# Kernel optimization log

Measured on AMD Instinct MI355X. Metric: run time of the kernel, lower is better.

## Reference

```python
import jax, jax.numpy as jnp
import numpy as np

HEADS = 4
DIM_HEAD = 32
DIM = 128
HIDDEN = HEADS * DIM_HEAD  # 128
SCALE = DIM_HEAD ** -0.5


def setup_inputs() -> dict:
    key = jax.random.key(0)
    ks = jax.random.split(key, 7)
    b, c, h, w = 4, DIM, 256, 256
    x = jax.random.normal(ks[0], (b, c, h, w), dtype=jnp.float32)
    context = jax.random.normal(ks[1], (b, c, h, w), dtype=jnp.float32)
    # conv1x1 weights stored as [out, in] matrices
    s_in = 1.0 / np.sqrt(DIM)
    Wq = jax.random.uniform(ks[2], (HIDDEN, DIM), jnp.float32, -s_in, s_in)
    Wk = jax.random.uniform(ks[3], (HIDDEN, DIM), jnp.float32, -s_in, s_in)
    Wv = jax.random.uniform(ks[4], (HIDDEN, DIM), jnp.float32, -s_in, s_in)
    s_h = 1.0 / np.sqrt(HIDDEN)
    Wo = jax.random.uniform(ks[5], (DIM, HIDDEN), jnp.float32, -s_h, s_h)
    bo = jax.random.uniform(ks[6], (DIM,), jnp.float32, -s_h, s_h)
    return {"x": x, "context": context, "Wq": Wq, "Wk": Wk, "Wv": Wv, "Wo": Wo, "bo": bo}


def reference(x, context, Wq, Wk, Wv, Wo, bo):
    b, c, h, w = x.shape
    n = h * w
    xf = x.reshape(b, c, n)         # flatten spatial
    cf = context.reshape(b, c, n)
    # conv1x1 projections == channel matmuls
    q = jnp.einsum('oc,bcn->bon', Wq, xf).reshape(b, HEADS, DIM_HEAD, n)
    k = jnp.einsum('oc,bcn->bon', Wk, cf).reshape(b, HEADS, DIM_HEAD, n)
    v = jnp.einsum('oc,bcn->bon', Wv, cf).reshape(b, HEADS, DIM_HEAD, n)
    q = q * SCALE
    k = jax.nn.softmax(k, axis=-1)  # softmax over spatial positions
    ctx = jnp.einsum('bhdn,bhen->bhde', k, v)   # [b,h,d,e] small d_head x d_head
    out = jnp.einsum('bhde,bhdn->bhen', ctx, q)  # [b,h,e,n]
    out = out.reshape(b, HIDDEN, n)
    out = jnp.einsum('oc,bcn->bon', Wo, out) + bo[None, :, None]
    return out.reshape(b, c, h, w)
```

## Files before the change

### kernel.cpp

```cpp
#include <hip/hip_runtime.h>
#include <cstdint>
#include <cstddef>

typedef __bf16 bf16x8 __attribute__((ext_vector_type(8)));
typedef float f32x4 __attribute__((ext_vector_type(4)));
typedef unsigned int u32x4 __attribute__((ext_vector_type(4)));
typedef unsigned int u32x2 __attribute__((ext_vector_type(2)));

#define MFMA16(a, b, c) __builtin_amdgcn_mfma_f32_16x16x32_bf16((a), (b), (c), 0, 0, 0)

static constexpr int CD = 128;
static constexpr int NTOK = 65536;
static constexpr float F_SCALE = 0.17677669529663688f;
static constexpr float F_LOG2E = 1.4426950408889634f;
static constexpr int PART = 4224;

__device__ __forceinline__ void gload_lds16(const float* g, void* l) {
  __builtin_amdgcn_global_load_lds(
      (const __attribute__((address_space(1))) void*)g,
      (__attribute__((address_space(3))) void*)l, 16, 0, 0);
}

__device__ __forceinline__ unsigned short bfb(float f) {
  return __builtin_bit_cast(unsigned short, (__bf16)f);
}
__device__ __forceinline__ unsigned pk2(float a, float b) {
  return (unsigned)bfb(a) | ((unsigned)bfb(b) << 16);
}

__device__ __forceinline__ void stage_swz(const float* src_base, float* T1,
                                          int w, int lg, int l15) {
#pragma unroll
  for (int i = 0; i < 8; ++i) {
    int c0 = w * 32 + i * 4;
    int row = c0 + lg;
    int g = l15 ^ ((row >> 3) & 3);
    gload_lds16(src_base + (size_t)row * NTOK + g * 4, (void*)(T1 + c0 * 64));
  }
}

__device__ __forceinline__ void transpose_vec(const float* T1, char* T2, int tid) {
  const int co = tid >> 4;
  const int nq = tid & 15;
  const int lgl = co & 3;
  f32x4 M[8];
#pragma unroll
  for (int i = 0; i < 8; ++i)
    M[i] = *(const f32x4*)(T1 + (co * 8 + i) * 64 + ((nq ^ lgl) * 4));
#pragma unroll
  for (int j = 0; j < 4; ++j) {
    int n = nq * 4 + j;
    u32x4 pk;
#pragma unroll
    for (int p = 0; p < 4; ++p)
      pk[p] = pk2(M[2 * p][j], M[2 * p + 1][j]);
    *(u32x4*)(T2 + n * 256 + ((co * 16) ^ ((n & 7) << 4))) = pk;
  }
}

__global__ __launch_bounds__(256, 2) void k1_ctx(
    const float* __restrict__ ctx_in, const float* __restrict__ Wk,
    const float* __restrict__ Wv, float* __restrict__ S_part,
    int cpb_log2, int nstrips) {
  __shared__ char smem[80 * 1024];
  float* T1 = (float*)smem;
  char* T2 = smem + 32 * 1024;
  char* EV = smem + 48 * 1024;

  const int tid = threadIdx.x;
  const int lane = tid & 63;
  const int w = tid >> 6;
  const int l15 = lane & 15;
  const int lg = lane >> 4;
  const int b = blockIdx.x >> cpb_log2;
  const int cb = blockIdx.x & ((1 << cpb_log2) - 1);

  bf16x8 Wf[4][4];
#pragma unroll
  for (int m = 0; m < 4; ++m) {
    const float* Wp = (m < 2) ? Wk : Wv;
    const float sc = (m < 2) ? F_LOG2E : 1.0f;
    int row = w * 32 + (m & 1) * 16 + l15;
#pragma unroll
    for (int ks = 0; ks < 4; ++ks) {
      const float* p = Wp + row * CD + ks * 32 + lg * 8;
#pragma unroll
      for (int e = 0; e < 8; ++e) Wf[m][ks][e] = (__bf16)(p[e] * sc);
    }
  }

  f32x4 Sacc[2][2];
#pragma unroll
  for (int i = 0; i < 2; ++i)
#pragma unroll
    for (int j = 0; j < 2; ++j) Sacc[i][j] = f32x4{0.f, 0.f, 0.f, 0.f};
  float zacc[2] = {0.f, 0.f};

  const float* src0 = ctx_in + (size_t)b * CD * NTOK + (size_t)cb * (nstrips * 64);
  const int xorr = (l15 & 7) << 4;
  char* Ew = EV + w * 8192;
  char* Vw = EV + w * 8192 + 4096;

  stage_swz(src0, T1, w, lg, l15);

  for (int s = 0; s < nstrips; ++s) {
    asm volatile("s_waitcnt vmcnt(0)" ::: "memory");
    __syncthreads();
    transpose_vec(T1, T2, tid);
    __syncthreads();
    if (s + 1 < nstrips) stage_swz(src0 + (s + 1) * 64, T1, w, lg, l15);

    f32x4 acc[4][4];
#pragma unroll
    for (int m = 0; m < 4; ++m)
#pragma unroll
      for (int t = 0; t < 4; ++t) acc[m][t] = f32x4{0.f, 0.f, 0.f, 0.f};
#pragma unroll
    for (int ks = 0; ks < 4; ++ks) {
      bf16x8 At[4];
#pragma unroll
      for (int t = 0; t < 4; ++t) {
        int n = t * 16 + l15;
        At[t] = *(const bf16x8*)(T2 + n * 256 + ((ks * 64 + lg * 16) ^ xorr));
      }
#pragma unroll
      for (int m = 0; m < 4; ++m)
#pragma unroll
        for (int t = 0; t < 4; ++t) acc[m][t] = MFMA16(At[t], Wf[m][ks], acc[m][t]);
    }

#pragma unroll
    for (int m = 0; m < 2; ++m) {
      int d = m * 16 + l15;
      int dx = (d & 7) << 4;
#pragma unroll
      for (int t = 0; t < 4; ++t) {
        f32x4 a = acc[m][t];
        float e0 = __builtin_exp2f(a[0]), e1 = __builtin_exp2f(a[1]);
        float e2 = __builtin_exp2f(a[2]), e3 = __builtin_exp2f(a[3]);
        zacc[m] += (e0 + e1) + (e2 + e3);
        u32x2 pe{pk2(e0, e1), pk2(e2, e3)};
        *(u32x2*)(Ew + d * 128 + ((t * 32 + lg * 8) ^ dx)) = pe;
        f32x4 v = acc[m + 2][t];
        u32x2 pv{pk2(v[0], v[1]), pk2(v[2], v[3])};
        *(u32x2*)(Vw + d * 128 + ((t * 32 + lg * 8) ^ dx)) = pv;
      }
    }

#pragma unroll
    for (int s2 = 0; s2 < 2; ++s2) {
      bf16x8 Ea[2], Vb[2];
#pragma unroll
      for (int md = 0; md < 2; ++md) {
        int d = md * 16 + l15;
        int off = (s2 * 64 + lg * 16) ^ ((d & 7) << 4);
        Ea[md] = *(const bf16x8*)(Ew + d * 128 + off);
        Vb[md] = *(const bf16x8*)(Vw + d * 128 + off);
      }
#pragma unroll
      for (int md = 0; md < 2; ++md)
#pragma unroll
        for (int ne = 0; ne < 2; ++ne) Sacc[md][ne] = MFMA16(Ea[md], Vb[ne], Sacc[md][ne]);
    }
  }

  float* outp = S_part + (size_t)blockIdx.x * PART;
#pragma unroll
  for (int md = 0; md < 2; ++md)
#pragma unroll
    for (int ne = 0; ne < 2; ++ne) {
      int e = ne * 16 + l15, d0 = md * 16 + lg * 4;
      *(f32x4*)(outp + w * 1024 + e * 32 + d0) = Sacc[md][ne];
    }
#pragma unroll
  for (int m = 0; m < 2; ++m) {
    float z = zacc[m];
    z += __shfl_xor(z, 16, 64);
    z += __shfl_xor(z, 32, 64);
    if (lg == 0) outp[4096 + w * 32 + m * 16 + l15] = z;
  }
}

__global__ void k2a_reduce(const float* __restrict__ S_part, float* __restrict__ S_red,
                           float* __restrict__ Z_red, int nparts) {
  int bid = blockIdx.x;
  int b = bid / 33, bs = bid % 33;
  int tid = threadIdx.x;
  __shared__ float red[256];
  int e_loc = tid & 127, half = tid >> 7;
  const float* base =
      S_part + (size_t)b * nparts * PART + (bs < 32 ? bs * 128 + e_loc : 4096 + e_loc);
  float sum = 0.f;
  int h = nparts >> 1;
  for (int p = half * h; p < half * h + h; ++p) sum += base[(size_t)p * PART];
  red[tid] = sum;
  __syncthreads();
  if (tid < 128) {
    float v = red[tid] + red[tid + 128];
    if (bs < 32)
      S_red[b * 4096 + bs * 128 + tid] = v;
    else
      Z_red[b * 128 + tid] = v;
  }
}

__global__ void k2b_weff(const float* __restrict__ S_red, const float* __restrict__ Z_red,
                         const float* __restrict__ Wq, const float* __restrict__ Wo,
                         float* __restrict__ W_eff) {
  int b = blockIdx.x >> 3, og = blockIdx.x & 7;
  int tid = threadIdx.x;
  __shared__ float ctx_lds[4096];
  __shared__ float T_lds[16 * 128];
  for (int i = tid * 16; i < tid * 16 + 16; ++i) {
    int hh = i >> 10, dd = i & 31;
    ctx_lds[i] = S_red[b * 4096 + i] / Z_red[b * 128 + hh * 32 + dd];
  }
  __syncthreads();
  {
    int o_loc = tid >> 4, hd0 = (tid & 15) * 8;
    int o = og * 16 + o_loc;
    for (int j = 0; j < 8; ++j) {
      int hd = hd0 + j, h = hd >> 5, d = hd & 31;
      const float* wo = Wo + o * 128 + h * 32;
      const float* cx = ctx_lds + h * 1024 + d;
      float acc = 0.f;
      for (int e = 0; e < 32; ++e) acc += wo[e] * cx[e * 32];
      T_lds[o_loc * 128 + hd] = acc;
    }
  }
  __syncthreads();
  {
    int o_loc = tid >> 4, c0 = (tid & 15) * 8;
    float acc[8] = {};
    const float* Trow = T_lds + o_loc * 128;
    for (int hd = 0; hd < 128; ++hd) {
      float tv = Trow[hd];
      const float* wq = Wq + hd * 128 + c0;
#pragma unroll
      for (int j = 0; j < 8; ++j) acc[j] += tv * wq[j];
    }
    float* op = W_eff + b * 16384 + (og * 16 + o_loc) * 128 + c0;
#pragma unroll
    for (int j = 0; j < 8; ++j) op[j] = F_SCALE * acc[j];
  }
}

__global__ __launch_bounds__(256, 3) void k3_out(const float* __restrict__ x,
                                                 const float* __restrict__ W_eff,
                                                 const float* __restrict__ bo,
                                                 float* __restrict__ out) {
  __shared__ char smem[48 * 1024];
  float* T1 = (float*)smem;
  char* T2 = smem + 32 * 1024;
  const int tid = threadIdx.x;
  const int lane = tid & 63;
  const int w = tid >> 6;
  const int l15 = lane & 15;
  const int lg = lane >> 4;
  const int b = blockIdx.x >> 8;
  const int cb = blockIdx.x & 255;

  bf16x8 Wf[2][4];
#pragma unroll
  for (int m = 0; m < 2; ++m) {
    int o = w * 32 + m * 16 + l15;
#pragma unroll
    for (int ks = 0; ks < 4; ++ks) {
      const float* p = W_eff + b * 16384 + o * 128 + ks * 32 + lg * 8;
#pragma unroll
      for (int e = 0; e < 8; ++e) Wf[m][ks][e] = (__bf16)p[e];
    }
  }
  float bof[2] = {bo[w * 32 + l15], bo[w * 32 + 16 + l15]};

  const float* src0 = x + (size_t)b * CD * NTOK + cb * 256;
  float* out0 = out + (size_t)b * CD * NTOK + cb * 256;
  const int xorr = (l15 & 7) << 4;

  stage_swz(src0, T1, w, lg, l15);

  for (int s = 0; s < 4; ++s) {
    asm volatile("s_waitcnt vmcnt(0)" ::: "memory");
    __syncthreads();
    transpose_vec(T1, T2, tid);
    __syncthreads();
    if (s + 1 < 4) stage_swz(src0 + (s + 1) * 64, T1, w, lg, l15);

    f32x4 acc[2][4];
#pragma unroll
    for (int m = 0; m < 2; ++m)
#pragma unroll
      for (int t = 0; t < 4; ++t) acc[m][t] = f32x4{0.f, 0.f, 0.f, 0.f};
#pragma unroll
    for (int ks = 0; ks < 4; ++ks) {
      bf16x8 At[4];
#pragma unroll
      for (int t = 0; t < 4; ++t) {
        int n = t * 16 + l15;
        At[t] = *(const bf16x8*)(T2 + n * 256 + ((ks * 64 + lg * 16) ^ xorr));
      }
#pragma unroll
      for (int m = 0; m < 2; ++m)
#pragma unroll
        for (int t = 0; t < 4; ++t) acc[m][t] = MFMA16(At[t], Wf[m][ks], acc[m][t]);
    }
#pragma unroll
    for (int m = 0; m < 2; ++m) {
      int o = w * 32 + m * 16 + l15;
#pragma unroll
      for (int t = 0; t < 4; ++t) {
        f32x4 v = acc[m][t];
        v[0] += bof[m]; v[1] += bof[m]; v[2] += bof[m]; v[3] += bof[m];
        *(f32x4*)(out0 + (size_t)o * NTOK + s * 64 + t * 16 + lg * 4) = v;
      }
    }
  }
}

extern "C" void kernel_launch(void* const* d_in, const int* in_sizes, int n_in,
                              void* d_out, int out_size, void* d_ws, size_t ws_size,
                              hipStream_t stream) {
  const float* x = (const float*)d_in[0];
  const float* ctxg = (const float*)d_in[1];
  const float* Wq = (const float*)d_in[2];
  const float* Wk = (const float*)d_in[3];
  const float* Wv = (const float*)d_in[4];
  const float* Wo = (const float*)d_in[5];
  const float* bo = (const float*)d_in[6];
  float* out = (float*)d_out;

  size_t need256 = ((size_t)1024 * PART + 16384 + 512 + 65536) * sizeof(float);
  int cpb_log2, nstrips;
  if (ws_size >= need256) { cpb_log2 = 8; nstrips = 4; }
  else                    { cpb_log2 = 7; nstrips = 8; }
  int nblk1 = 4 << cpb_log2;

  float* ws = (float*)d_ws;
  float* S_part = ws;
  float* S_red = ws + (size_t)nblk1 * PART;
  float* Z_red = S_red + 16384;
  float* W_eff = Z_red + 512;

  k1_ctx<<<dim3(nblk1), dim3(256), 0, stream>>>(ctxg, Wk, Wv, S_part, cpb_log2, nstrips);
  k2a_reduce<<<dim3(132), dim3(256), 0, stream>>>(S_part, S_red, Z_red, 1 << cpb_log2);
  k2b_weff<<<dim3(32), dim3(256), 0, stream>>>(S_red, Z_red, Wq, Wo, W_eff);
  k3_out<<<dim3(1024), dim3(256), 0, stream>>>(x, W_eff, bo, out);
}
```

Baseline: 164.9 us.

## Replace LDS-staged transpose with register-prefetched strips and per-wave output tiling

Both streaming kernels drop the global_load_lds staging buffer and the block-wide transpose pass. Each wave now loads its strip straight into registers, prefetching the next strip, and packs bf16 pairs directly into a transposed LDS tile. k1 uses a double-buffered tile with a single barrier per strip. k3 becomes per-wave with no block barriers: each wave computes all 128 output channels for 16 tokens and stages results through LDS so the global stores are coalesced. The grid is fixed at 512 blocks and the partial-sum layout changes, with k2b adjusted to match; this costs more registers (8x4 weight fragments in k3) and uses narrower 4-byte LDS writes.

```diff
diff --git a/kernel.cpp b/kernel.cpp
--- a/kernel.cpp
+++ b/kernel.cpp
@@ -4,7 +4,6 @@
 
 typedef __bf16 bf16x8 __attribute__((ext_vector_type(8)));
 typedef float f32x4 __attribute__((ext_vector_type(4)));
-typedef unsigned int u32x4 __attribute__((ext_vector_type(4)));
 typedef unsigned int u32x2 __attribute__((ext_vector_type(2)));
 
 #define MFMA16(a, b, c) __builtin_amdgcn_mfma_f32_16x16x32_bf16((a), (b), (c), 0, 0, 0)
@@ -14,66 +13,53 @@
 static constexpr float F_SCALE = 0.17677669529663688f;
 static constexpr float F_LOG2E = 1.4426950408889634f;
 static constexpr int PART = 4224;
-
-__device__ __forceinline__ void gload_lds16(const float* g, void* l) {
-  __builtin_amdgcn_global_load_lds(
-      (const __attribute__((address_space(1))) void*)g,
-      (__attribute__((address_space(3))) void*)l, 16, 0, 0);
-}
-
-__device__ __forceinline__ unsigned short bfb(float f) {
-  return __builtin_bit_cast(unsigned short, (__bf16)f);
-}
+static constexpr int NPARTS = 128;
+
 __device__ __forceinline__ unsigned pk2(float a, float b) {
-  return (unsigned)bfb(a) | ((unsigned)bfb(b) << 16);
-}
-
-__device__ __forceinline__ void stage_swz(const float* src_base, float* T1,
-                                          int w, int lg, int l15) {
-#pragma unroll
-  for (int i = 0; i < 8; ++i) {
-    int c0 = w * 32 + i * 4;
-    int row = c0 + lg;
-    int g = l15 ^ ((row >> 3) & 3);
-    gload_lds16(src_base + (size_t)row * NTOK + g * 4, (void*)(T1 + c0 * 64));
-  }
-}
-
-__device__ __forceinline__ void transpose_vec(const float* T1, char* T2, int tid) {
-  const int co = tid >> 4;
-  const int nq = tid & 15;
-  const int lgl = co & 3;
-  f32x4 M[8];
-#pragma unroll
-  for (int i = 0; i < 8; ++i)
-    M[i] = *(const f32x4*)(T1 + (co * 8 + i) * 64 + ((nq ^ lgl) * 4));
-#pragma unroll
-  for (int j = 0; j < 4; ++j) {
-    int n = nq * 4 + j;
-    u32x4 pk;
-#pragma unroll
-    for (int p = 0; p < 4; ++p)
-      pk[p] = pk2(M[2 * p][j], M[2 * p + 1][j]);
-    *(u32x4*)(T2 + n * 256 + ((co * 16) ^ ((n & 7) << 4))) = pk;
-  }
+  unsigned short ua = __builtin_bit_cast(unsigned short, (__bf16)a);
+  unsigned short ub = __builtin_bit_cast(unsigned short, (__bf16)b);
+  return (unsigned)ua | ((unsigned)ub << 16);
+}
+
+struct Frag { f32x4 A[4]; f32x4 B[4]; };
+
+__device__ __forceinline__ Frag load_strip(const float* src, int lane) {
+  Frag f;
+#pragma unroll
+  for (int u = 0; u < 4; ++u) {
+    const float* p = src + (size_t)(u * 32 + (lane >> 2) * 2) * NTOK + (lane & 3) * 4;
+    f.A[u] = *(const f32x4*)p;
+    f.B[u] = *(const f32x4*)(p + NTOK);
+  }
+  return f;
+}
+
+__device__ __forceinline__ void pack_write(const Frag& f, char* T2row, int lane) {
+#pragma unroll
+  for (int u = 0; u < 4; ++u)
+#pragma unroll
+    for (int j = 0; j < 4; ++j) {
+      int n = (lane & 3) * 4 + j;
+      int cp = u * 16 + (lane >> 2);
+      *(unsigned*)(T2row + n * 256 + ((cp * 4) ^ ((n & 7) << 4))) =
+          pk2(f.A[u][j], f.B[u][j]);
+    }
 }
 
 __global__ __launch_bounds__(256, 2) void k1_ctx(
     const float* __restrict__ ctx_in, const float* __restrict__ Wk,
-    const float* __restrict__ Wv, float* __restrict__ S_part,
-    int cpb_log2, int nstrips) {
-  __shared__ char smem[80 * 1024];
-  float* T1 = (float*)smem;
-  char* T2 = smem + 32 * 1024;
-  char* EV = smem + 48 * 1024;
-
+    const float* __restrict__ Wv, float* __restrict__ S_part) {
+  __shared__ char smem[64 * 1024];
   const int tid = threadIdx.x;
   const int lane = tid & 63;
   const int w = tid >> 6;
   const int l15 = lane & 15;
   const int lg = lane >> 4;
-  const int b = blockIdx.x >> cpb_log2;
-  const int cb = blockIdx.x & ((1 << cpb_log2) - 1);
+  const int b = blockIdx.x >> 7;
+  const int cb = blockIdx.x & 127;
+
+  char* Eb = smem + 32 * 1024 + w * 8192;
+  char* Vb = Eb + 4096;
 
   bf16x8 Wf[4][4];
 #pragma unroll
@@ -96,19 +82,16 @@
     for (int j = 0; j < 2; ++j) Sacc[i][j] = f32x4{0.f, 0.f, 0.f, 0.f};
   float zacc[2] = {0.f, 0.f};
 
-  const float* src0 = ctx_in + (size_t)b * CD * NTOK + (size_t)cb * (nstrips * 64);
-  const int xorr = (l15 & 7) << 4;
-  char* Ew = EV + w * 8192;
-  char* Vw = EV + w * 8192 + 4096;
-
-  stage_swz(src0, T1, w, lg, l15);
-
-  for (int s = 0; s < nstrips; ++s) {
-    asm volatile("s_waitcnt vmcnt(0)" ::: "memory");
+  const float* src = ctx_in + (size_t)b * CD * NTOK + cb * 512 + w * 16;
+
+  Frag f = load_strip(src, lane);
+#pragma unroll
+  for (int s = 0; s < 8; ++s) {
+    Frag fn;
+    if (s < 7) fn = load_strip(src + (s + 1) * 64, lane);
+    char* T2 = smem + (s & 1) * 16384;
+    pack_write(f, T2 + w * 4096, lane);
     __syncthreads();
-    transpose_vec(T1, T2, tid);
-    __syncthreads();
-    if (s + 1 < nstrips) stage_swz(src0 + (s + 1) * 64, T1, w, lg, l15);
 
     f32x4 acc[4][4];
 #pragma unroll
@@ -119,10 +102,9 @@
     for (int ks = 0; ks < 4; ++ks) {
       bf16x8 At[4];
 #pragma unroll
-      for (int t = 0; t < 4; ++t) {
-        int n = t * 16 + l15;
-        At[t] = *(const bf16x8*)(T2 + n * 256 + ((ks * 64 + lg * 16) ^ xorr));
-      }
+      for (int t = 0; t < 4; ++t)
+        At[t] = *(const bf16x8*)(T2 + (t * 16 + l15) * 256 +
+                                 ((ks * 64 + lg * 16) ^ ((l15 & 7) << 4)));
 #pragma unroll
       for (int m = 0; m < 4; ++m)
 #pragma unroll
@@ -139,39 +121,38 @@
         float e0 = __builtin_exp2f(a[0]), e1 = __builtin_exp2f(a[1]);
         float e2 = __builtin_exp2f(a[2]), e3 = __builtin_exp2f(a[3]);
         zacc[m] += (e0 + e1) + (e2 + e3);
-        u32x2 pe{pk2(e0, e1), pk2(e2, e3)};
-        *(u32x2*)(Ew + d * 128 + ((t * 32 + lg * 8) ^ dx)) = pe;
+        *(u32x2*)(Eb + d * 128 + ((t * 32 + lg * 8) ^ dx)) =
+            u32x2{pk2(e0, e1), pk2(e2, e3)};
         f32x4 v = acc[m + 2][t];
-        u32x2 pv{pk2(v[0], v[1]), pk2(v[2], v[3])};
-        *(u32x2*)(Vw + d * 128 + ((t * 32 + lg * 8) ^ dx)) = pv;
+        *(u32x2*)(Vb + d * 128 + ((t * 32 + lg * 8) ^ dx)) =
+            u32x2{pk2(v[0], v[1]), pk2(v[2], v[3])};
       }
     }
 
 #pragma unroll
     for (int s2 = 0; s2 < 2; ++s2) {
-      bf16x8 Ea[2], Vb[2];
+      bf16x8 Ea[2], Vv[2];
 #pragma unroll
       for (int md = 0; md < 2; ++md) {
         int d = md * 16 + l15;
-        int off = (s2 * 64 + lg * 16) ^ ((d & 7) << 4);
-        Ea[md] = *(const bf16x8*)(Ew + d * 128 + off);
-        Vb[md] = *(const bf16x8*)(Vw + d * 128 + off);
+        int off = d * 128 + ((s2 * 64 + lg * 16) ^ ((d & 7) << 4));
+        Ea[md] = *(const bf16x8*)(Eb + off);
+        Vv[md] = *(const bf16x8*)(Vb + off);
       }
 #pragma unroll
       for (int md = 0; md < 2; ++md)
 #pragma unroll
-        for (int ne = 0; ne < 2; ++ne) Sacc[md][ne] = MFMA16(Ea[md], Vb[ne], Sacc[md][ne]);
-    }
+        for (int ne = 0; ne < 2; ++ne) Sacc[md][ne] = MFMA16(Ea[md], Vv[ne], Sacc[md][ne]);
+    }
+    if (s < 7) f = fn;
   }
 
   float* outp = S_part + (size_t)blockIdx.x * PART;
 #pragma unroll
   for (int md = 0; md < 2; ++md)
 #pragma unroll
-    for (int ne = 0; ne < 2; ++ne) {
-      int e = ne * 16 + l15, d0 = md * 16 + lg * 4;
-      *(f32x4*)(outp + w * 1024 + e * 32 + d0) = Sacc[md][ne];
-    }
+    for (int ne = 0; ne < 2; ++ne)
+      *(f32x4*)(outp + w * 1024 + (md * 2 + ne) * 256 + lane * 4) = Sacc[md][ne];
 #pragma unroll
   for (int m = 0; m < 2; ++m) {
     float z = zacc[m];
@@ -182,16 +163,16 @@
 }
 
 __global__ void k2a_reduce(const float* __restrict__ S_part, float* __restrict__ S_red,
-                           float* __restrict__ Z_red, int nparts) {
+                           float* __restrict__ Z_red) {
   int bid = blockIdx.x;
   int b = bid / 33, bs = bid % 33;
   int tid = threadIdx.x;
   __shared__ float red[256];
   int e_loc = tid & 127, half = tid >> 7;
   const float* base =
-      S_part + (size_t)b * nparts * PART + (bs < 32 ? bs * 128 + e_loc : 4096 + e_loc);
+      S_part + (size_t)b * NPARTS * PART + (bs < 32 ? bs * 128 + e_loc : 4096 + e_loc);
   float sum = 0.f;
-  int h = nparts >> 1;
+  int h = NPARTS >> 1;
   for (int p = half * h; p < half * h + h; ++p) sum += base[(size_t)p * PART];
   red[tid] = sum;
   __syncthreads();
@@ -212,8 +193,10 @@
   __shared__ float ctx_lds[4096];
   __shared__ float T_lds[16 * 128];
   for (int i = tid * 16; i < tid * 16 + 16; ++i) {
-    int hh = i >> 10, dd = i & 31;
-    ctx_lds[i] = S_red[b * 4096 + i] / Z_red[b * 128 + hh * 32 + dd];
+    int h = i >> 10, d = (i >> 5) & 31, e = i & 31;
+    int fl = h * 1024 + (((d >> 4) * 2 + (e >> 4)) << 8) + (((d >> 2) & 3) << 6) +
+             ((e & 15) << 2) + (d & 3);
+    ctx_lds[i] = S_red[b * 4096 + fl] / Z_red[b * 128 + h * 32 + d];
   }
   __syncthreads();
   {
@@ -222,9 +205,9 @@
     for (int j = 0; j < 8; ++j) {
       int hd = hd0 + j, h = hd >> 5, d = hd & 31;
       const float* wo = Wo + o * 128 + h * 32;
-      const float* cx = ctx_lds + h * 1024 + d;
+      const float* cx = ctx_lds + h * 1024 + d * 32;
       float acc = 0.f;
-      for (int e = 0; e < 32; ++e) acc += wo[e] * cx[e * 32];
+      for (int e = 0; e < 32; ++e) acc += wo[e] * cx[e];
       T_lds[o_loc * 128 + hd] = acc;
     }
   }
@@ -245,25 +228,26 @@
   }
 }
 
-__global__ __launch_bounds__(256, 3) void k3_out(const float* __restrict__ x,
+__global__ __launch_bounds__(256, 2) void k3_out(const float* __restrict__ x,
                                                  const float* __restrict__ W_eff,
                                                  const float* __restrict__ bo,
                                                  float* __restrict__ out) {
-  __shared__ char smem[48 * 1024];
-  float* T1 = (float*)smem;
-  char* T2 = smem + 32 * 1024;
+  __shared__ char smem[32 * 1024];
   const int tid = threadIdx.x;
   const int lane = tid & 63;
   const int w = tid >> 6;
   const int l15 = lane & 15;
   const int lg = lane >> 4;
-  const int b = blockIdx.x >> 8;
-  const int cb = blockIdx.x & 255;
-
-  bf16x8 Wf[2][4];
-#pragma unroll
-  for (int m = 0; m < 2; ++m) {
-    int o = w * 32 + m * 16 + l15;
+  const int b = blockIdx.x >> 7;
+  const int cb = blockIdx.x & 127;
+
+  char* T2 = smem + w * 8192;
+  char* Dt = smem + w * 8192;
+
+  bf16x8 Wf[8][4];
+#pragma unroll
+  for (int m = 0; m < 8; ++m) {
+    int o = m * 16 + l15;
 #pragma unroll
     for (int ks = 0; ks < 4; ++ks) {
       const float* p = W_eff + b * 16384 + o * 128 + ks * 32 + lg * 8;
@@ -271,49 +255,45 @@
       for (int e = 0; e < 8; ++e) Wf[m][ks][e] = (__bf16)p[e];
     }
   }
-  float bof[2] = {bo[w * 32 + l15], bo[w * 32 + 16 + l15]};
-
-  const float* src0 = x + (size_t)b * CD * NTOK + cb * 256;
-  float* out0 = out + (size_t)b * CD * NTOK + cb * 256;
-  const int xorr = (l15 & 7) << 4;
-
-  stage_swz(src0, T1, w, lg, l15);
-
-  for (int s = 0; s < 4; ++s) {
-    asm volatile("s_waitcnt vmcnt(0)" ::: "memory");
-    __syncthreads();
-    transpose_vec(T1, T2, tid);
-    __syncthreads();
-    if (s + 1 < 4) stage_swz(src0 + (s + 1) * 64, T1, w, lg, l15);
-
-    f32x4 acc[2][4];
-#pragma unroll
-    for (int m = 0; m < 2; ++m)
-#pragma unroll
-      for (int t = 0; t < 4; ++t) acc[m][t] = f32x4{0.f, 0.f, 0.f, 0.f};
+  float bof[8];
+#pragma unroll
+  for (int m = 0; m < 8; ++m) bof[m] = bo[m * 16 + l15];
+
+  const float* src = x + (size_t)b * CD * NTOK + cb * 512 + w * 128;
+  float* dst = out + (size_t)b * CD * NTOK + cb * 512 + w * 128;
+
+  Frag f = load_strip(src, lane);
+#pragma unroll
+  for (int s = 0; s < 8; ++s) {
+    Frag fn;
+    if (s < 7) fn = load_strip(src + (s + 1) * 16, lane);
+    pack_write(f, T2, lane);
+
+    f32x4 acc[8];
+#pragma unroll
+    for (int m = 0; m < 8; ++m) acc[m] = f32x4{0.f, 0.f, 0.f, 0.f};
 #pragma unroll
     for (int ks = 0; ks < 4; ++ks) {
-      bf16x8 At[4];
-#pragma unroll
-      for (int t = 0; t < 4; ++t) {
-        int n = t * 16 + l15;
-        At[t] = *(const bf16x8*)(T2 + n * 256 + ((ks * 64 + lg * 16) ^ xorr));
-      }
-#pragma unroll
-      for (int m = 0; m < 2; ++m)
-#pragma unroll
-        for (int t = 0; t < 4; ++t) acc[m][t] = MFMA16(At[t], Wf[m][ks], acc[m][t]);
-    }
-#pragma unroll
-    for (int m = 0; m < 2; ++m) {
-      int o = w * 32 + m * 16 + l15;
-#pragma unroll
-      for (int t = 0; t < 4; ++t) {
-        f32x4 v = acc[m][t];
-        v[0] += bof[m]; v[1] += bof[m]; v[2] += bof[m]; v[3] += bof[m];
-        *(f32x4*)(out0 + (size_t)o * NTOK + s * 64 + t * 16 + lg * 4) = v;
-      }
-    }
+      bf16x8 At = *(const bf16x8*)(T2 + l15 * 256 + ((ks * 64 + lg * 16) ^ ((l15 & 7) << 4)));
+#pragma unroll
+      for (int m = 0; m < 8; ++m) acc[m] = MFMA16(At, Wf[m][ks], acc[m]);
+    }
+
+#pragma unroll
+    for (int m = 0; m < 8; ++m) {
+      int o = m * 16 + l15;
+      f32x4 v = acc[m];
+      v[0] += bof[m]; v[1] += bof[m]; v[2] += bof[m]; v[3] += bof[m];
+      *(f32x4*)(Dt + o * 64 + ((lg * 16) ^ (((o >> 1) & 3) << 4))) = v;
+    }
+#pragma unroll
+    for (int i = 0; i < 8; ++i) {
+      int o2 = i * 16 + (lane >> 2);
+      int nq = lane & 3;
+      f32x4 v = *(const f32x4*)(Dt + o2 * 64 + ((nq * 16) ^ (((o2 >> 1) & 3) << 4)));
+      *(f32x4*)(dst + (size_t)o2 * NTOK + s * 16 + nq * 4) = v;
+    }
+    if (s < 7) f = fn;
   }
 }
 
@@ -329,20 +309,14 @@
   const float* bo = (const float*)d_in[6];
   float* out = (float*)d_out;
 
-  size_t need256 = ((size_t)1024 * PART + 16384 + 512 + 65536) * sizeof(float);
-  int cpb_log2, nstrips;
-  if (ws_size >= need256) { cpb_log2 = 8; nstrips = 4; }
-  else                    { cpb_log2 = 7; nstrips = 8; }
-  int nblk1 = 4 << cpb_log2;
-
   float* ws = (float*)d_ws;
   float* S_part = ws;
-  float* S_red = ws + (size_t)nblk1 * PART;
+  float* S_red = ws + (size_t)512 * PART;
   float* Z_red = S_red + 16384;
   float* W_eff = Z_red + 512;
 
-  k1_ctx<<<dim3(nblk1), dim3(256), 0, stream>>>(ctxg, Wk, Wv, S_part, cpb_log2, nstrips);
-  k2a_reduce<<<dim3(132), dim3(256), 0, stream>>>(S_part, S_red, Z_red, 1 << cpb_log2);
+  k1_ctx<<<dim3(512), dim3(256), 0, stream>>>(ctxg, Wk, Wv, S_part);
+  k2a_reduce<<<dim3(132), dim3(256), 0, stream>>>(S_part, S_red, Z_red);
   k2b_weff<<<dim3(32), dim3(256), 0, stream>>>(S_red, Z_red, Wq, Wo, W_eff);
-  k3_out<<<dim3(1024), dim3(256), 0, stream>>>(x, W_eff, bo, out);
-}
+  k3_out<<<dim3(512), dim3(256), 0, stream>>>(x, W_eff, bo, out);
+}
```

New measurement: 240.1 us. +45.6%, slower.
